# Optimization experiments

Measured on AMD Instinct MI355X. Metric: run time of the kernel, lower is better.

## Reference

```python
import jax, jax.numpy as jnp
import numpy as np

B, N, H, F, DIN, NC = 4, 1024, 8, 256, 256, 10  # batch graphs, nodes, heads, feat/head, input dim, classes


def setup_inputs() -> dict:
    key = jax.random.key(0)
    ks = jax.random.split(key, 12)
    def rn(k, shape, s=0.05):
        return jax.random.normal(k, shape, jnp.float32) * s
    return dict(
        features=rn(ks[0], (B, N, DIN), 1.0),
        eigvects=rn(ks[1], (B, N, DIN), 1.0),  # unused by forward, mirrors original signature
        attn_mask=jnp.zeros((B, N, N), jnp.float32),  # additive mask: 0 = edge, -inf = no edge
        W1=rn(ks[2], (DIN, H * F)), a_src1=rn(ks[3], (H, F)), a_tgt1=rn(ks[4], (H, F)),
        skip1=rn(ks[5], (DIN, H * F)), b1=jnp.zeros((H * F,), jnp.float32),
        W2=rn(ks[6], (H * F, H * F)), a_src2=rn(ks[7], (H, F)), a_tgt2=rn(ks[8], (H, F)),
        skip2=rn(ks[9], (H * F, H * F)), b2=jnp.zeros((F,), jnp.float32),
        Wc=rn(ks[10], (F, NC)), bc=jnp.zeros((NC,), jnp.float32),
    )


def _gat_layer(x, mask, W, a_s, a_t, skipW, b, concat):
    # GAT IMP2: dense all-pairs scores + additive connectivity mask. Dropout is eval-mode identity.
    Bb, Nn, _ = x.shape
    Hh, Ff = a_s.shape
    p = (x @ W).reshape(Bb, Nn, Hh, Ff)                      # projected node features (B,N,H,F)
    s_src = jnp.einsum('bnhf,hf->bnh', p, a_s)
    s_tgt = jnp.einsum('bnhf,hf->bnh', p, a_t)
    # score[b,i,j,h] = leaky(src_i + tgt_j) + mask[b,i,j]
    scores = jax.nn.leaky_relu(s_src[:, :, None, :] + s_tgt[:, None, :, :], 0.2) + mask[..., None]
    attn = jax.nn.softmax(scores, axis=2)                    # softmax over neighbors j
    out = jnp.einsum('bijh,bjhf->bihf', attn, p)
    out = out + (x @ skipW).reshape(Bb, Nn, Hh, Ff)          # skip connection (projected)
    out = out.reshape(Bb, Nn, Hh * Ff) if concat else out.mean(axis=2)
    out = out + b
    return jax.nn.elu(out) if concat else out


def reference(features, eigvects, attn_mask, W1, a_src1, a_tgt1, skip1, b1,
              W2, a_src2, a_tgt2, skip2, b2, Wc, bc):
    x = _gat_layer(features, attn_mask, W1, a_src1, a_tgt1, skip1, b1, True)   # (B,N,H*F), ELU
    x = _gat_layer(x, attn_mask, W2, a_src2, a_tgt2, skip2, b2, False)         # (B,N,F), heads averaged
    g = x.mean(axis=1)                                                         # mean pool over nodes
    return g @ Wc + bc                                                         # (B, n_classes)
```

## Files before the change

### kernel.cpp

```cpp
#include <hip/hip_runtime.h>
#include <hip/hip_bf16.h>
#include <stdint.h>
#include <stddef.h>

typedef __hip_bfloat16 bf16;
typedef __attribute__((ext_vector_type(8))) short bhalf8;
typedef __attribute__((ext_vector_type(4))) short short4v;
typedef __attribute__((ext_vector_type(4))) float floatx4;

static __device__ __forceinline__ float b2f(bf16 v) { return __bfloat162float(v); }
static __device__ __forceinline__ bf16  f2b(float v) { return __float2bfloat16(v); }
static __device__ __forceinline__ short f2s(float v) {
    union { bf16 b; short s; } u; u.b = __float2bfloat16(v); return u.s;
}
static __device__ __forceinline__ float s2f(short v) {
    union { short s; bf16 b; } u; u.s = v; return b2f(u.b);
}

static __device__ __forceinline__ float loadf(const void* p, size_t i, int f32) {
    return f32 ? ((const float*)p)[i] : b2f(((const bf16*)p)[i]);
}

static __device__ __forceinline__ void gl_lds16(const void* g, void* l) {
    __builtin_amdgcn_global_load_lds(
        (const __attribute__((address_space(1))) void*)g,
        (__attribute__((address_space(3))) void*)l, 16, 0, 0);
}

static __device__ __forceinline__ void load_mask4b(const bf16* m, size_t idx,
                                                   float* mv) {
    short4v v = *(const short4v*)(m + idx);
    #pragma unroll
    for (int t = 0; t < 4; t++) mv[t] = s2f(v[t]);
}

__global__ __launch_bounds__(256) void prep_k(const void* __restrict__ feat,
                                              bf16* __restrict__ featc,
                                              const void* __restrict__ mask,
                                              bf16* __restrict__ maskb,
                                              float* __restrict__ zbase, int nzero,
                                              const void* __restrict__ W1,
                                              bf16* __restrict__ W1t,
                                              const void* __restrict__ skip1,
                                              bf16* __restrict__ S1t,
                                              const void* __restrict__ W2,
                                              const void* __restrict__ a_src1,
                                              const void* __restrict__ a_tgt1,
                                              const void* __restrict__ a_src2,
                                              const void* __restrict__ a_tgt2,
                                              bf16* __restrict__ Wa1b,
                                              bf16* __restrict__ Wa2b,
                                              int* __restrict__ flagp)
{
    __shared__ int sflag;
    __shared__ bf16 tile[32][33];
    const int tid = threadIdx.x;

    if (tid < 64) {
        const unsigned short* s = (const unsigned short*)W1;
        int bad = 0;
        #pragma unroll
        for (int i = 0; i < 4; i++) {
            int e = (s[tid * 4 + i] >> 7) & 0xFF;
            if (e > 0x85 || (e != 0 && e < 0x60)) bad++;
        }
        bad += __shfl_xor(bad, 1, 64);
        bad += __shfl_xor(bad, 2, 64);
        bad += __shfl_xor(bad, 4, 64);
        bad += __shfl_xor(bad, 8, 64);
        bad += __shfl_xor(bad, 16, 64);
        bad += __shfl_xor(bad, 32, 64);
        if (tid == 0) sflag = (bad > 16) ? 1 : 0;
    }
    __syncthreads();
    const int f32 = sflag;

    int id = blockIdx.x;
    if (id == 0 && tid == 0) *flagp = f32;

    if (id < 4096) {
        const int i = id * 256 + tid;
        featc[i] = f32 ? f2b(((const float*)feat)[i]) : ((const bf16*)feat)[i];
        return;
    }
    id -= 4096;
    if (id < 4096) {
        const size_t i = (size_t)id * 1024 + tid * 4;
        if (f32) {
            float4 v = *(const float4*)((const float*)mask + i);
            short4v o;
            o[0] = f2s(v.x); o[1] = f2s(v.y); o[2] = f2s(v.z); o[3] = f2s(v.w);
            *(short4v*)(maskb + i) = o;
        } else {
            *(short4v*)(maskb + i) = *(const short4v*)((const bf16*)mask + i);
        }
        return;
    }
    id -= 4096;
    if (id < 480) {
        const int i = id * 256 + tid;
        if (i < nzero) zbase[i] = 0.f;
        return;
    }
    id -= 480;
    if (id < 1024) {
        const void* in = (id < 512) ? W1 : skip1;
        bf16* out = (id < 512) ? W1t : S1t;
        const int t = id & 511;
        const int bx = t & 63, byy = t >> 6;
        const int tx = tid & 31, ty = tid >> 5;
        const int c0 = bx * 32, r0 = byy * 32;
        #pragma unroll
        for (int yy = ty; yy < 32; yy += 8)
            tile[yy][tx] = f2b(loadf(in, (size_t)(r0 + yy) * 2048 + c0 + tx, f32));
        __syncthreads();
        #pragma unroll
        for (int yy = ty; yy < 32; yy += 8)
            out[(size_t)(c0 + yy) * 256 + r0 + tx] = tile[tx][yy];
        return;
    }
    id -= 1024;
    if (id < 512) {
        const int wave = tid >> 6, lane = tid & 63;
        const int base = id * 64;
        const int hh = base >> 11, h = hh & 7;
        const void* a = (hh < 8) ? a_src2 : a_tgt2;
        float av[4];
        #pragma unroll
        for (int i = 0; i < 4; i++) av[i] = loadf(a, h * 256 + lane * 4 + i, f32);
        #pragma unroll 4
        for (int o = 0; o < 16; o++) {
            const int idx = base + wave * 16 + o;
            const int k = idx & 2047;
            float acc = 0.f;
            #pragma unroll
            for (int i = 0; i < 4; i++)
                acc = fmaf(loadf(W2, (size_t)k * 2048 + h * 256 + lane * 4 + i, f32),
                           av[i], acc);
            #pragma unroll
            for (int off2 = 32; off2; off2 >>= 1) acc += __shfl_down(acc, off2, 64);
            if (lane == 0) Wa2b[idx] = f2b(acc);
        }
        return;
    }
    id -= 512;
    {
        const int wave = tid >> 6, lane = tid & 63;
        const int base = id * 64;
        const int hh = base >> 8, h = hh & 7;
        const void* a = (hh < 8) ? a_src1 : a_tgt1;
        float av[4];
        #pragma unroll
        for (int i = 0; i < 4; i++) av[i] = loadf(a, h * 256 + lane * 4 + i, f32);
        #pragma unroll 4
        for (int o = 0; o < 16; o++) {
            const int idx = base + wave * 16 + o;
            const int k = idx & 255;
            float acc = 0.f;
            #pragma unroll
            for (int i = 0; i < 4; i++)
                acc = fmaf(loadf(W1, (size_t)k * 2048 + h * 256 + lane * 4 + i, f32),
                           av[i], acc);
            #pragma unroll
            for (int off2 = 32; off2; off2 >>= 1) acc += __shfl_down(acc, off2, 64);
            if (lane == 0) Wa1b[idx] = f2b(acc);
        }
    }
}

__global__ __launch_bounds__(256) void gemm_dual(const bf16* __restrict__ featc,
                                                 const bf16* __restrict__ W1t,
                                                 const bf16* __restrict__ S1t,
                                                 bf16* __restrict__ pT,
                                                 bf16* __restrict__ sk1)
{
    __shared__ __align__(16) short sA[128][32];
    __shared__ __align__(16) short sB[128][32];
    const int tid = threadIdx.x;
    const int z = blockIdx.z;
    const bf16* A  = z ? featc : W1t;
    const bf16* Bt = z ? S1t   : featc;
    const int mbase = (z ? blockIdx.x : blockIdx.y) * 128;
    const int nbase = (z ? blockIdx.y : blockIdx.x) * 128;
    const int wave = tid >> 6, lane = tid & 63;
    const int wm = wave >> 1, wn = wave & 1;
    const int lrow = lane & 15, quad = lane >> 4;

    floatx4 acc[4][4];
    #pragma unroll
    for (int i = 0; i < 4; i++)
        #pragma unroll
        for (int j = 0; j < 4; j++)
            acc[i][j] = (floatx4){0.f, 0.f, 0.f, 0.f};

    const int srow = wave * 32 + (lane >> 2);
    const int scol = (lane & 3) * 8;
    const bf16* gA0 = A  + (size_t)(mbase + srow) * 256 + scol;
    const bf16* gA1 = gA0 + (size_t)16 * 256;
    const bf16* gB0 = Bt + (size_t)(nbase + srow) * 256 + scol;
    const bf16* gB1 = gB0 + (size_t)16 * 256;
    char* lA0 = (char*)&sA[0][0] + wave * 2048 + lane * 16;
    char* lA1 = lA0 + 1024;
    char* lB0 = (char*)&sB[0][0] + wave * 2048 + lane * 16;
    char* lB1 = lB0 + 1024;

    for (int k0 = 0; k0 < 256; k0 += 32) {
        __syncthreads();
        gl_lds16(gA0 + k0, lA0);
        gl_lds16(gA1 + k0, lA1);
        gl_lds16(gB0 + k0, lB0);
        gl_lds16(gB1 + k0, lB1);
        __syncthreads();
        bhalf8 af[4], bfr[4];
        #pragma unroll
        for (int t = 0; t < 4; t++) af[t]  = *(const bhalf8*)&sA[wm * 64 + t * 16 + lrow][quad * 8];
        #pragma unroll
        for (int t = 0; t < 4; t++) bfr[t] = *(const bhalf8*)&sB[wn * 64 + t * 16 + lrow][quad * 8];
        #pragma unroll
        for (int tm = 0; tm < 4; tm++)
            #pragma unroll
            for (int tn = 0; tn < 4; tn++)
                acc[tm][tn] = __builtin_amdgcn_mfma_f32_16x16x32_bf16(af[tm], bfr[tn], acc[tm][tn], 0, 0, 0);
    }

    #pragma unroll
    for (int tm = 0; tm < 4; tm++) {
        #pragma unroll
        for (int tn = 0; tn < 4; tn++) {
            const int col = nbase + wn * 64 + tn * 16 + lrow;
            #pragma unroll
            for (int r = 0; r < 4; r++) {
                const int row = mbase + wm * 64 + tm * 16 + quad * 4 + r;
                if (z) {
                    sk1[(size_t)row * 2048 + col] = f2b(acc[tm][tn][r]);
                } else {
                    const size_t idx = ((size_t)((col >> 10) * 8 + (row >> 8)) << 18)
                                     + (size_t)(row & 255) * 1024 + (col & 1023);
                    pT[idx] = f2b(acc[tm][tn][r]);
                }
            }
        }
    }
}

template <int K>
__global__ __launch_bounds__(256) void score_k(const bf16* __restrict__ X,
                                               const bf16* __restrict__ Wab,
                                               float* __restrict__ ss,
                                               float* __restrict__ st)
{
    constexpr int VPL = K / 64;
    const int wave = threadIdx.x >> 6, lane = threadIdx.x & 63;
    const int n = blockIdx.x * 4 + wave;
    const int b = n >> 10, nn = n & 1023;

    const bf16* xr = X + (size_t)n * K + lane * VPL;
    float xv[VPL];
    if (VPL == 4) {
        short4v v = *(const short4v*)xr;
        #pragma unroll
        for (int t = 0; t < 4; t++) xv[t] = s2f(v[t]);
    } else {
        #pragma unroll
        for (int c = 0; c < VPL / 8; c++) {
            bhalf8 v = *(const bhalf8*)(xr + c * 8);
            #pragma unroll
            for (int t = 0; t < 8; t++) xv[c * 8 + t] = s2f(v[t]);
        }
    }

    #pragma unroll
    for (int hh = 0; hh < 16; hh++) {
        const bf16* wr = Wab + (size_t)hh * K + lane * VPL;
        float acc = 0.f;
        if (VPL == 4) {
            short4v v = *(const short4v*)wr;
            #pragma unroll
            for (int t = 0; t < 4; t++) acc = fmaf(xv[t], s2f(v[t]), acc);
        } else {
            #pragma unroll
            for (int c = 0; c < VPL / 8; c++) {
                bhalf8 v = *(const bhalf8*)(wr + c * 8);
                #pragma unroll
                for (int t = 0; t < 8; t++) acc = fmaf(xv[c * 8 + t], s2f(v[t]), acc);
            }
        }
        #pragma unroll
        for (int off = 32; off; off >>= 1) acc += __shfl_down(acc, off, 64);
        if (lane == 0) {
            const int h = hh & 7;
            if (hh < 8) ss[(b * 8 + h) * 1024 + nn] = acc;
            else        st[(b * 8 + h) * 1024 + nn] = acc;
        }
    }
}

__global__ __launch_bounds__(256) void attn_fused(const float* __restrict__ s_src_t,
                                                  const float* __restrict__ s_tgt_t,
                                                  const bf16* __restrict__ maskb,
                                                  const bf16* __restrict__ pT,
                                                  const bf16* __restrict__ sk,
                                                  const void* __restrict__ bias,
                                                  bf16* __restrict__ x2,
                                                  const int* __restrict__ flag)
{
    __shared__ __align__(16) short sA[2][32][32];
    __shared__ __align__(16) short sB[2][256][32];
    __shared__ short sStgt[1024];
    __shared__ float sInvl[32];

    const int tid = threadIdx.x;
    const int by = blockIdx.x, bh = blockIdx.y;
    const int b = bh >> 3, h = bh & 7;
    const int f32 = *flag;
    const int wave = tid >> 6, lane = tid & 63;
    const int lrow = lane & 15, quad = lane >> 4;

    #pragma unroll
    for (int q = 0; q < 4; q++)
        sStgt[q * 256 + tid] = f2s(s_tgt_t[bh * 1024 + q * 256 + tid]);

    const int row  = tid >> 3;
    const int col0 = (tid & 7) * 4;
    const float ssr = s_src_t[bh * 1024 + by * 32 + row];
    const size_t mrow0 = ((size_t)(b * 1024 + by * 32 + row)) << 10;

    const bf16* gB = pT + ((size_t)bh << 18) + (size_t)(tid >> 2) * 1024 + (tid & 3) * 8;

    floatx4 acc[2][4];
    #pragma unroll
    for (int i = 0; i < 2; i++)
        #pragma unroll
        for (int j = 0; j < 4; j++)
            acc[i][j] = (floatx4){0.f, 0.f, 0.f, 0.f};

    float lacc = 0.f;

    auto stageB = [&](int k0, int buf) {
        const bf16* g = gB + k0;
        char* l = (char*)&sB[buf][0][0] + tid * 16;
        #pragma unroll
        for (int c = 0; c < 4; c++)
            gl_lds16(g + (size_t)(64 * c) * 1024, l + c * 4096);
    };
    auto genA = [&](int k0, int buf, const float* mv) {
        const short* sp = &sStgt[k0 + col0];
        short4v ev;
        #pragma unroll
        for (int t = 0; t < 4; t++) {
            float x = ssr + s2f(sp[t]);
            x = fmaxf(x, 0.2f * x);
            float e = __expf(x + mv[t]);
            lacc += e;
            ev[t] = f2s(e);
        }
        *(short4v*)&sA[buf][row][col0] = ev;
    };

    float mv[4];
    stageB(0, 0);
    load_mask4b(maskb, mrow0 + col0, mv);
    __syncthreads();
    genA(0, 0, mv);
    load_mask4b(maskb, mrow0 + 32 + col0, mv);

    int cur = 0;
    for (int k0 = 0; k0 < 1024; k0 += 32, cur ^= 1) {
        __syncthreads();
        if (k0 + 32 < 1024) {
            const int nxt = cur ^ 1;
            stageB(k0 + 32, nxt);
            genA(k0 + 32, nxt, mv);
            if (k0 + 64 < 1024)
                load_mask4b(maskb, mrow0 + k0 + 64 + col0, mv);
        }
        bhalf8 af[2], bfr[4];
        #pragma unroll
        for (int mt = 0; mt < 2; mt++)
            af[mt] = *(const bhalf8*)&sA[cur][mt * 16 + lrow][quad * 8];
        #pragma unroll
        for (int nt = 0; nt < 4; nt++)
            bfr[nt] = *(const bhalf8*)&sB[cur][wave * 64 + nt * 16 + lrow][quad * 8];
        #pragma unroll
        for (int mt = 0; mt < 2; mt++)
            #pragma unroll
            for (int nt = 0; nt < 4; nt++)
                acc[mt][nt] = __builtin_amdgcn_mfma_f32_16x16x32_bf16(af[mt], bfr[nt], acc[mt][nt], 0, 0, 0);
    }

    lacc += __shfl_xor(lacc, 1, 64);
    lacc += __shfl_xor(lacc, 2, 64);
    lacc += __shfl_xor(lacc, 4, 64);
    if ((tid & 7) == 0) sInvl[row] = 1.0f / lacc;
    __syncthreads();

    #pragma unroll
    for (int mt = 0; mt < 2; mt++) {
        #pragma unroll
        for (int r = 0; r < 4; r++) {
            const int rl = mt * 16 + quad * 4 + r;
            const int rg = by * 32 + rl;
            const float il = sInvl[rl];
            #pragma unroll
            for (int nt = 0; nt < 4; nt++) {
                const int col = wave * 64 + nt * 16 + lrow;
                const int hf = h * 256 + col;
                const size_t idx = ((size_t)(b * 1024 + rg)) * 2048 + hf;
                float v = acc[mt][nt][r] * il + b2f(sk[idx]) + loadf(bias, hf, f32);
                v = (v > 0.f) ? v : expm1f(v);
                x2[idx] = f2b(v);
            }
        }
    }
}

__global__ __launch_bounds__(256) void colsoft_k(const float* __restrict__ s_src_t,
                                                 const float* __restrict__ s_tgt_t,
                                                 const bf16* __restrict__ maskb,
                                                 float* __restrict__ c)
{
    __shared__ float sS[64];
    __shared__ float sIl[64];
    const int bh = blockIdx.x, iz = blockIdx.y, b = bh >> 3;
    const int tid = threadIdx.x;
    const int i0 = iz * 64;
    if (tid < 64) sS[tid] = s_src_t[bh * 1024 + i0 + tid];
    __syncthreads();

    {
        const int row = tid >> 2, c4 = tid & 3;
        const float ssr = sS[row];
        const size_t mrow = ((size_t)(b * 1024 + i0 + row)) << 10;
        float l = 0.f;
        #pragma unroll 4
        for (int q = 0; q < 64; q++) {
            const int j = c4 * 256 + q * 4;
            float mv[4];
            load_mask4b(maskb, mrow + j, mv);
            float4 s4 = *(const float4*)(s_tgt_t + bh * 1024 + j);
            float sv[4] = {s4.x, s4.y, s4.z, s4.w};
            #pragma unroll
            for (int t = 0; t < 4; t++) {
                float x = ssr + sv[t];
                x = fmaxf(x, 0.2f * x);
                l += __expf(x + mv[t]);
            }
        }
        l += __shfl_xor(l, 1, 64);
        l += __shfl_xor(l, 2, 64);
        if ((tid & 3) == 0) sIl[row] = 1.0f / l;
    }
    __syncthreads();

    const int j0 = tid * 4;
    float4 s4 = *(const float4*)(s_tgt_t + bh * 1024 + j0);
    float sv[4] = {s4.x, s4.y, s4.z, s4.w};
    float a[4] = {0.f, 0.f, 0.f, 0.f};
    #pragma unroll 4
    for (int r = 0; r < 64; r++) {
        const float sr = sS[r], il = sIl[r];
        float mv[4];
        load_mask4b(maskb, (((size_t)(b * 1024 + i0 + r)) << 10) + j0, mv);
        #pragma unroll
        for (int t = 0; t < 4; t++) {
            float x = sr + sv[t];
            x = fmaxf(x, 0.2f * x);
            a[t] = fmaf(il, __expf(x + mv[t]), a[t]);
        }
    }
    #pragma unroll
    for (int t = 0; t < 4; t++)
        atomicAdd(&c[bh * 1024 + j0 + t], a[t]);
}

__global__ __launch_bounds__(256) void yx_k(const bf16* __restrict__ x2,
                                            const float* __restrict__ c,
                                            float* __restrict__ y,
                                            float* __restrict__ xbar)
{
    __shared__ float sC[8][32];
    const int b = blockIdx.x, kt = blockIdx.y, jc = blockIdx.z;
    const int t = threadIdx.x;
    const int k = kt * 256 + t;
    const int j0 = jc * 32;
    {
        const int h = t >> 5, jj = t & 31;
        sC[h][jj] = c[(b * 8 + h) * 1024 + j0 + jj];
    }
    __syncthreads();
    float acc[8] = {0.f, 0.f, 0.f, 0.f, 0.f, 0.f, 0.f, 0.f};
    float ax = 0.f;
    #pragma unroll 4
    for (int jj = 0; jj < 32; jj++) {
        const float xv = b2f(x2[((size_t)(b * 1024 + j0 + jj)) * 2048 + k]);
        ax += xv;
        #pragma unroll
        for (int h = 0; h < 8; h++) acc[h] = fmaf(sC[h][jj], xv, acc[h]);
    }
    #pragma unroll
    for (int h = 0; h < 8; h++)
        atomicAdd(&y[(b * 8 + h) * 2048 + k], acc[h]);
    atomicAdd(&xbar[b * 2048 + k], ax);
}

__global__ __launch_bounds__(256) void gs_k(const void* __restrict__ W2,
                                            const void* __restrict__ skip2,
                                            const float* __restrict__ y,
                                            const float* __restrict__ xbar,
                                            float* __restrict__ gA,
                                            float* __restrict__ gS,
                                            const int* __restrict__ flagp)
{
    __shared__ float sY[64];
    const int f32 = *flagp;
    int id = blockIdx.x;
    if (id < 1024) {
        const int bh = id & 31, kc = id >> 5;
        const int h = bh & 7, f = threadIdx.x;
        const int k0 = kc * 64;
        if (threadIdx.x < 64) sY[threadIdx.x] = y[bh * 2048 + k0 + threadIdx.x];
        __syncthreads();
        float acc = 0.f;
        #pragma unroll 4
        for (int kk = 0; kk < 64; kk++)
            acc = fmaf(sY[kk], loadf(W2, (size_t)(k0 + kk) * 2048 + h * 256 + f, f32), acc);
        atomicAdd(&gA[bh * 256 + f], acc);
    } else {
        const int idx = id - 1024;
        const int b = idx & 3, hft = (idx >> 2) & 7, kc = idx >> 5;
        const int hf = hft * 256 + threadIdx.x;
        const int k0 = kc * 64;
        if (threadIdx.x < 64) sY[threadIdx.x] = xbar[b * 2048 + k0 + threadIdx.x];
        __syncthreads();
        float acc = 0.f;
        #pragma unroll 4
        for (int kk = 0; kk < 64; kk++)
            acc = fmaf(sY[kk], loadf(skip2, (size_t)(k0 + kk) * 2048 + hf, f32), acc);
        atomicAdd(&gS[b * 2048 + hf], acc);
    }
}

__global__ __launch_bounds__(256) void classify2_k(const float* __restrict__ gA,
                                                   const float* __restrict__ gS,
                                                   const void* __restrict__ b2,
                                                   const void* __restrict__ Wc,
                                                   const void* __restrict__ bc,
                                                   void* __restrict__ out,
                                                   const int* __restrict__ flag)
{
    __shared__ float gv[256];
    const int f32 = *flag;
    const int b = blockIdx.x, f = threadIdx.x;
    float s = 0.f;
    #pragma unroll
    for (int h = 0; h < 8; h++)
        s += gA[(b * 8 + h) * 256 + f] + gS[b * 2048 + h * 256 + f];
    gv[f] = s * (1.0f / 8192.0f) + loadf(b2, f, f32);
    __syncthreads();
    if (f < 10) {
        float acc = loadf(bc, f, f32);
        for (int k = 0; k < 256; k++)
            acc = fmaf(gv[k], loadf(Wc, k * 10 + f, f32), acc);
        if (f32) ((float*)out)[b * 10 + f] = acc;
        else     ((bf16*)out)[b * 10 + f] = f2b(acc);
    }
}

extern "C" void kernel_launch(void* const* d_in, const int* in_sizes, int n_in,
                              void* d_out, int out_size, void* d_ws, size_t ws_size,
                              hipStream_t stream)
{
    (void)in_sizes; (void)n_in; (void)out_size; (void)ws_size;
    const void* feat   = d_in[0];
    const void* mask   = d_in[2];
    const void* W1     = d_in[3];
    const void* a_src1 = d_in[4];
    const void* a_tgt1 = d_in[5];
    const void* skip1  = d_in[6];
    const void* b1     = d_in[7];
    const void* W2     = d_in[8];
    const void* a_src2 = d_in[9];
    const void* a_tgt2 = d_in[10];
    const void* skip2  = d_in[11];
    const void* b2v    = d_in[12];
    const void* Wc     = d_in[13];
    const void* bc     = d_in[14];

    char* ws = (char*)d_ws;
    size_t off = 0;
    auto alloc = [&](size_t bytes) -> void* {
        void* p = ws + off;
        off += (bytes + 255) & ~(size_t)255;
        return p;
    };
    int*   flag  = (int*)alloc(256);
    bf16*  featc = (bf16*)alloc(4096ull * 256 * 2);
    bf16*  maskb = (bf16*)alloc(4ull * 1024 * 1024 * 2);
    bf16*  W1t   = (bf16*)alloc(2048ull * 256 * 2);
    bf16*  S1t   = (bf16*)alloc(2048ull * 256 * 2);
    bf16*  sk1   = (bf16*)alloc(4096ull * 2048 * 2);
    bf16*  x2    = (bf16*)alloc(4096ull * 2048 * 2);
    bf16*  pT    = (bf16*)alloc(4096ull * 2048 * 2);
    float* ss    = (float*)alloc(32ull * 1024 * 4);
    float* st    = (float*)alloc(32ull * 1024 * 4);
    bf16*  Wa1b  = (bf16*)alloc(16ull * 256 * 2);
    bf16*  Wa2b  = (bf16*)alloc(16ull * 2048 * 2);
    float* cbuf = (float*)alloc(32ull * 1024 * 4);
    float* gA   = (float*)alloc(32ull * 256 * 4);
    float* gS   = (float*)alloc(4ull * 2048 * 4);
    float* xbar = (float*)alloc(4ull * 2048 * 4);
    float* y    = (float*)alloc(32ull * 2048 * 4);
    const int nzero = 32768 + 3 * 8192 + 65536;

    prep_k<<<10272, 256, 0, stream>>>(feat, featc, mask, maskb, cbuf, nzero,
                                      W1, W1t, skip1, S1t, W2,
                                      a_src1, a_tgt1, a_src2, a_tgt2,
                                      Wa1b, Wa2b, flag);
    gemm_dual<<<dim3(32, 16, 2), 256, 0, stream>>>(featc, W1t, S1t, pT, sk1);
    score_k<256><<<1024, 256, 0, stream>>>(featc, Wa1b, ss, st);
    attn_fused<<<dim3(32, 32), 256, 0, stream>>>(ss, st, maskb, pT, sk1, b1, x2, flag);
    score_k<2048><<<1024, 256, 0, stream>>>(x2, Wa2b, ss, st);
    colsoft_k<<<dim3(32, 16), 256, 0, stream>>>(ss, st, maskb, cbuf);
    yx_k<<<dim3(4, 8, 32), 256, 0, stream>>>(x2, cbuf, y, xbar);
    gs_k<<<2048, 256, 0, stream>>>(W2, skip2, y, xbar, gA, gS, flag);
    classify2_k<<<4, 256, 0, stream>>>(gA, gS, b2v, Wc, bc, d_out, flag);
}
```

Before: 350.0 us.

## Deepen mask prefetch, split colsoft rows finer, share weight loads across batch in gs_k

In attn_fused, mask values are now prefetched two K-steps ahead with double register buffers, so the mask load latency has more time to hide. colsoft_k processes 32 rows per block instead of 64, which doubles the grid for more parallelism at the cost of more atomic adds to the column sums. gs_k is restructured so each block reads one slice of W2/skip2 rows and applies it to all 4 batches at once, cutting redundant weight reads by 4x while keeping the same grid size with smaller K chunks.

Result: no change. 352.9 us (+0.9%).

```diff
diff --git a/kernel.cpp b/kernel.cpp
--- a/kernel.cpp
+++ b/kernel.cpp
@@ -357,12 +357,13 @@
         *(short4v*)&sA[buf][row][col0] = ev;
     };
 
-    float mv[4];
+    float mv0[4], mv1[4];
     stageB(0, 0);
-    load_mask4b(maskb, mrow0 + col0, mv);
-    __syncthreads();
-    genA(0, 0, mv);
-    load_mask4b(maskb, mrow0 + 32 + col0, mv);
+    load_mask4b(maskb, mrow0 + col0, mv0);
+    __syncthreads();
+    genA(0, 0, mv0);
+    load_mask4b(maskb, mrow0 + 32 + col0, mv0);
+    load_mask4b(maskb, mrow0 + 64 + col0, mv1);
 
     int cur = 0;
     for (int k0 = 0; k0 < 1024; k0 += 32, cur ^= 1) {
@@ -370,9 +371,11 @@
         if (k0 + 32 < 1024) {
             const int nxt = cur ^ 1;
             stageB(k0 + 32, nxt);
-            genA(k0 + 32, nxt, mv);
-            if (k0 + 64 < 1024)
-                load_mask4b(maskb, mrow0 + k0 + 64 + col0, mv);
+            genA(k0 + 32, nxt, mv0);
+            #pragma unroll
+            for (int t = 0; t < 4; t++) mv0[t] = mv1[t];
+            if (k0 + 96 < 1024)
+                load_mask4b(maskb, mrow0 + k0 + 96 + col0, mv1);
         }
         bhalf8 af[2], bfr[4];
         #pragma unroll
@@ -419,22 +422,22 @@
                                                  const bf16* __restrict__ maskb,
                                                  float* __restrict__ c)
 {
-    __shared__ float sS[64];
-    __shared__ float sIl[64];
+    __shared__ float sS[32];
+    __shared__ float sIl[32];
     const int bh = blockIdx.x, iz = blockIdx.y, b = bh >> 3;
     const int tid = threadIdx.x;
-    const int i0 = iz * 64;
-    if (tid < 64) sS[tid] = s_src_t[bh * 1024 + i0 + tid];
+    const int i0 = iz * 32;
+    if (tid < 32) sS[tid] = s_src_t[bh * 1024 + i0 + tid];
     __syncthreads();
 
     {
-        const int row = tid >> 2, c4 = tid & 3;
+        const int row = tid >> 3, c8 = tid & 7;
         const float ssr = sS[row];
         const size_t mrow = ((size_t)(b * 1024 + i0 + row)) << 10;
         float l = 0.f;
         #pragma unroll 4
-        for (int q = 0; q < 64; q++) {
-            const int j = c4 * 256 + q * 4;
+        for (int q = 0; q < 32; q++) {
+            const int j = c8 * 128 + q * 4;
             float mv[4];
             load_mask4b(maskb, mrow + j, mv);
             float4 s4 = *(const float4*)(s_tgt_t + bh * 1024 + j);
@@ -448,7 +451,8 @@
         }
         l += __shfl_xor(l, 1, 64);
         l += __shfl_xor(l, 2, 64);
-        if ((tid & 3) == 0) sIl[row] = 1.0f / l;
+        l += __shfl_xor(l, 4, 64);
+        if ((tid & 7) == 0) sIl[row] = 1.0f / l;
     }
     __syncthreads();
 
@@ -457,7 +461,7 @@
     float sv[4] = {s4.x, s4.y, s4.z, s4.w};
     float a[4] = {0.f, 0.f, 0.f, 0.f};
     #pragma unroll 4
-    for (int r = 0; r < 64; r++) {
+    for (int r = 0; r < 32; r++) {
         const float sr = sS[r], il = sIl[r];
         float mv[4];
         load_mask4b(maskb, (((size_t)(b * 1024 + i0 + r)) << 10) + j0, mv);
@@ -511,32 +515,35 @@
                                             float* __restrict__ gS,
                                             const int* __restrict__ flagp)
 {
-    __shared__ float sY[64];
+    __shared__ float sV[4][16];
     const int f32 = *flagp;
     int id = blockIdx.x;
-    if (id < 1024) {
-        const int bh = id & 31, kc = id >> 5;
-        const int h = bh & 7, f = threadIdx.x;
-        const int k0 = kc * 64;
-        if (threadIdx.x < 64) sY[threadIdx.x] = y[bh * 2048 + k0 + threadIdx.x];
-        __syncthreads();
-        float acc = 0.f;
-        #pragma unroll 4
-        for (int kk = 0; kk < 64; kk++)
-            acc = fmaf(sY[kk], loadf(W2, (size_t)(k0 + kk) * 2048 + h * 256 + f, f32), acc);
-        atomicAdd(&gA[bh * 256 + f], acc);
+    const int gam = (id < 1024) ? 1 : 0;
+    if (!gam) id -= 1024;
+    const int h = id & 7, kc = id >> 3;
+    const int k0 = kc * 16, f = threadIdx.x;
+    if (threadIdx.x < 64) {
+        const int bb = threadIdx.x >> 4, kk = threadIdx.x & 15;
+        sV[bb][kk] = gam ? y[(bb * 8 + h) * 2048 + k0 + kk]
+                         : xbar[bb * 2048 + k0 + kk];
+    }
+    __syncthreads();
+    const void* W = gam ? W2 : skip2;
+    float acc[4] = {0.f, 0.f, 0.f, 0.f};
+    #pragma unroll 4
+    for (int kk = 0; kk < 16; kk++) {
+        const float w = loadf(W, (size_t)(k0 + kk) * 2048 + h * 256 + f, f32);
+        #pragma unroll
+        for (int bb = 0; bb < 4; bb++) acc[bb] = fmaf(sV[bb][kk], w, acc[bb]);
+    }
+    if (gam) {
+        #pragma unroll
+        for (int bb = 0; bb < 4; bb++)
+            atomicAdd(&gA[(bb * 8 + h) * 256 + f], acc[bb]);
     } else {
-        const int idx = id - 1024;
-        const int b = idx & 3, hft = (idx >> 2) & 7, kc = idx >> 5;
-        const int hf = hft * 256 + threadIdx.x;
-        const int k0 = kc * 64;
-        if (threadIdx.x < 64) sY[threadIdx.x] = xbar[b * 2048 + k0 + threadIdx.x];
-        __syncthreads();
-        float acc = 0.f;
-        #pragma unroll 4
-        for (int kk = 0; kk < 64; kk++)
-            acc = fmaf(sY[kk], loadf(skip2, (size_t)(k0 + kk) * 2048 + hf, f32), acc);
-        atomicAdd(&gS[b * 2048 + hf], acc);
+        #pragma unroll
+        for (int bb = 0; bb < 4; bb++)
+            atomicAdd(&gS[bb * 2048 + h * 256 + f], acc[bb]);
     }
 }
 
@@ -620,7 +627,7 @@
     score_k<256><<<1024, 256, 0, stream>>>(featc, Wa1b, ss, st);
     attn_fused<<<dim3(32, 32), 256, 0, stream>>>(ss, st, maskb, pT, sk1, b1, x2, flag);
     score_k<2048><<<1024, 256, 0, stream>>>(x2, Wa2b, ss, st);
-    colsoft_k<<<dim3(32, 16), 256, 0, stream>>>(ss, st, maskb, cbuf);
+    colsoft_k<<<dim3(32, 32), 256, 0, stream>>>(ss, st, maskb, cbuf);
     yx_k<<<dim3(4, 8, 32), 256, 0, stream>>>(x2, cbuf, y, xbar);
     gs_k<<<2048, 256, 0, stream>>>(W2, skip2, y, xbar, gA, gS, flag);
     classify2_k<<<4, 256, 0, stream>>>(gA, gS, b2v, Wc, bc, d_out, flag);
```
